# Kernel tuning notes

Measured on AMD Instinct MI355X. Metric: run time of the kernel, lower is better.

## Reference

```python
import jax, jax.numpy as jnp
import numpy as np
import math

L, B, T, C, H, DH, V, MEM = 6, 2, 1024, 1024, 16, 64, 32000, 128

def _ln(x, g, b):
    m = jnp.mean(x, -1, keepdims=True)
    v = jnp.mean((x - m) ** 2, -1, keepdims=True)
    return (x - m) * jax.lax.rsqrt(v + 1e-5) * g + b

def _rel_shift(x):
    # x: [B,H,Q,K]; TransformerXL shift trick: pad zero col, reshape, drop first row
    b, h, q, k = x.shape
    xp = jnp.pad(x, ((0, 0), (0, 0), (0, 0), (1, 0)))
    xp = xp.reshape(b, h, k + 1, q)
    return xp[:, :, 1:, :].reshape(b, h, q, k)

def setup_inputs():
    key = jax.random.key(0)
    ks = jax.random.split(key, 12)
    d = {}
    d['idx'] = jax.random.randint(ks[0], (B, T), 0, V)
    d['mems'] = jax.random.normal(ks[1], (L, B, MEM, C), dtype=jnp.float32) * 0.02
    d['wte'] = jax.random.normal(ks[2], (V, C), dtype=jnp.float32) * 0.02
    d['ln1_g'] = jnp.ones((L, C), jnp.float32); d['ln1_b'] = jnp.zeros((L, C), jnp.float32)
    d['attn_w'] = jax.random.normal(ks[3], (L, C, 3 * C), dtype=jnp.float32) * 0.02
    d['attn_b'] = jnp.zeros((L, 3 * C), jnp.float32)
    d['proj_w'] = jax.random.normal(ks[4], (L, C, C), dtype=jnp.float32) * 0.02
    d['proj_b'] = jnp.zeros((L, C), jnp.float32)
    d['r_emb'] = jax.random.normal(ks[5], (L, H, DH), dtype=jnp.float32) * 0.02
    d['r_bias'] = jax.random.normal(ks[6], (L, H, DH), dtype=jnp.float32) * 0.02
    d['ln2_g'] = jnp.ones((L, C), jnp.float32); d['ln2_b'] = jnp.zeros((L, C), jnp.float32)
    d['fc_w'] = jax.random.normal(ks[7], (L, C, 4 * C), dtype=jnp.float32) * 0.02
    d['fc_b'] = jnp.zeros((L, 4 * C), jnp.float32)
    d['fc2_w'] = jax.random.normal(ks[8], (L, 4 * C, C), dtype=jnp.float32) * 0.02
    d['fc2_b'] = jnp.zeros((L, C), jnp.float32)
    d['lnf_g'] = jnp.ones((C,), jnp.float32); d['lnf_b'] = jnp.zeros((C,), jnp.float32)
    d['lm_w'] = jax.random.normal(ks[9], (C, V), dtype=jnp.float32) * 0.02
    return d

def _attn(x, mem, w, b, pw, pb, remb, rbias):
    Bx, Tx, Cx = x.shape
    cat = jnp.concatenate([mem, x], axis=1)          # [B,K,C], K = mem_len + Tx
    K = cat.shape[1]
    qkv = cat @ w + b
    q, k, v = jnp.split(qkv, 3, axis=-1)
    q = q.reshape(Bx, K, H, DH).transpose(0, 2, 1, 3)
    k = k.reshape(Bx, K, H, DH).transpose(0, 2, 1, 3)
    v = v.reshape(Bx, K, H, DH).transpose(0, 2, 1, 3)
    q = q + rbias[None, :, None, :]
    AC = jnp.einsum('bhid,bhjd->bhij', q, k)
    # BD: r is r_emb broadcast over positions, so q@r^T is constant over j
    s = jnp.einsum('bhid,hd->bhi', q, remb)
    BD = _rel_shift(jnp.broadcast_to(s[..., None], (Bx, H, K, K)))
    p = jax.nn.softmax((AC + BD) / math.sqrt(DH), axis=-1)
    y = jnp.einsum('bhij,bhjd->bhid', p, v).transpose(0, 2, 1, 3).reshape(Bx, K, Cx)
    y = y @ pw + pb
    new_mem = cat[:, -MEM:]
    return y, new_mem

def reference(idx, mems, wte, ln1_g, ln1_b, attn_w, attn_b, proj_w, proj_b, r_emb, r_bias, ln2_g, ln2_b, fc_w, fc_b, fc2_w, fc2_b, lnf_g, lnf_b, lm_w):
    x = wte[idx]                                      # [B,T,C]
    new_mems = []
    for l in range(L):
        h = _ln(x, ln1_g[l], ln1_b[l])
        y, nm = _attn(h, mems[l], attn_w[l], attn_b[l], proj_w[l], proj_b[l], r_emb[l], r_bias[l])
        h2 = _ln(y, ln2_g[l], ln2_b[l])
        m = jax.nn.gelu(h2 @ fc_w[l] + fc_b[l], approximate=False) @ fc2_w[l] + fc2_b[l]
        x = y + m                                     # note: residual onto attn output (length grows by MEM per layer)
        new_mems.append(nm)
    x = _ln(x, lnf_g, lnf_b)
    logits = x @ lm_w                                 # [B, L*MEM+T, V]
    return logits, jnp.stack(new_mems)
```

## Files before the change

### kernel.cpp

```cpp
#include <hip/hip_runtime.h>
#include <hip/hip_bf16.h>
#include <hip/hip_fp16.h>

#define LNUM 6
#define BB 2
#define TT 1024
#define CC 1024
#define HH 16
#define DHH 64
#define VV 32000
#define MM 128

typedef _Float16 f16;
typedef _Float16 f16x8 __attribute__((ext_vector_type(8)));
typedef float f32x4 __attribute__((ext_vector_type(4)));

__device__ __forceinline__ void g2lds16(const void* g, void* l) {
    __builtin_amdgcn_global_load_lds((const __attribute__((address_space(1))) void*)g,
                                     (__attribute__((address_space(3))) void*)l,
                                     16, 0, 0);
}

__device__ __forceinline__ float wred(float v) {
#pragma unroll
    for (int o = 32; o > 0; o >>= 1) v += __shfl_xor(v, o);
    return v;
}

__global__ __launch_bounds__(256)
void transpose_k(const float* __restrict__ W, f16* __restrict__ WT, int R, int Cc)
{
    __shared__ float tile[64][65];
    const size_t base = (size_t)blockIdx.z * R * Cc;
    const int c0 = blockIdx.x * 64, r0 = blockIdx.y * 64;
    const int tx = threadIdx.x & 15, ty = threadIdx.x >> 4;
#pragma unroll
    for (int i = 0; i < 4; ++i) {
        const int row = ty + i * 16;
        float4 v = *(const float4*)&W[base + (size_t)(r0 + row) * Cc + c0 + tx * 4];
        tile[row][tx * 4 + 0] = v.x;
        tile[row][tx * 4 + 1] = v.y;
        tile[row][tx * 4 + 2] = v.z;
        tile[row][tx * 4 + 3] = v.w;
    }
    __syncthreads();
#pragma unroll
    for (int i = 0; i < 4; ++i) {
        const int c = ty + i * 16;
        union { f16 h4[4]; uint2 u; } pk;
        pk.h4[0] = (f16)tile[tx * 4 + 0][c];
        pk.h4[1] = (f16)tile[tx * 4 + 1][c];
        pk.h4[2] = (f16)tile[tx * 4 + 2][c];
        pk.h4[3] = (f16)tile[tx * 4 + 3][c];
        *(uint2*)&WT[base + (size_t)(c0 + c) * R + r0 + tx * 4] = pk.u;
    }
}

__global__ __launch_bounds__(256)
void embed_k(const int* __restrict__ idx, const float* __restrict__ wte, float* __restrict__ X)
{
    const int row = blockIdx.x;
    const int id = idx[row];
    const float4* src = (const float4*)(wte + (size_t)id * CC);
    float4* dst = (float4*)(X + (size_t)row * CC);
    dst[threadIdx.x] = src[threadIdx.x];
}

__global__ __launch_bounds__(256)
void ln_k(const float* __restrict__ X, const float* __restrict__ g,
          const float* __restrict__ bta, f16* __restrict__ outH)
{
    const int row = blockIdx.x * 4 + (threadIdx.x >> 6);
    const int lane = threadIdx.x & 63;
    const float4* xr = (const float4*)(X + (size_t)row * CC);
    float4 v[4];
    float s = 0.f;
#pragma unroll
    for (int i = 0; i < 4; ++i) { v[i] = xr[i * 64 + lane]; s += v[i].x + v[i].y + v[i].z + v[i].w; }
    s = wred(s);
    const float mean = s * (1.f / CC);
    float q = 0.f;
#pragma unroll
    for (int i = 0; i < 4; ++i) {
        float a = v[i].x - mean, b = v[i].y - mean, c = v[i].z - mean, d = v[i].w - mean;
        q += a * a + b * b + c * c + d * d;
    }
    q = wred(q);
    const float rs = rsqrtf(q * (1.f / CC) + 1e-5f);
    const float4* g4 = (const float4*)g;
    const float4* b4 = (const float4*)bta;
    uint2* orow = (uint2*)(outH + (size_t)row * CC);
#pragma unroll
    for (int i = 0; i < 4; ++i) {
        float4 gg = g4[i * 64 + lane], bb = b4[i * 64 + lane];
        union { f16 h4[4]; uint2 u; } pk;
        pk.h4[0] = (f16)((v[i].x - mean) * rs * gg.x + bb.x);
        pk.h4[1] = (f16)((v[i].y - mean) * rs * gg.y + bb.y);
        pk.h4[2] = (f16)((v[i].z - mean) * rs * gg.z + bb.z);
        pk.h4[3] = (f16)((v[i].w - mean) * rs * gg.w + bb.w);
        orow[i * 64 + lane] = pk.u;
    }
}

__global__ __launch_bounds__(256)
void ln1cat_k(const float* __restrict__ X, const float* __restrict__ memsL,
              const float* __restrict__ g, const float* __restrict__ bta,
              f16* __restrict__ catH, float* __restrict__ nmOut,
              int K, int Kin)
{
    const int row = blockIdx.x * 4 + (threadIdx.x >> 6);
    const int lane = threadIdx.x & 63;
    const int b = row / K, rr = row % K;
    uint2* crow = (uint2*)(catH + (size_t)row * CC);
    if (rr < MM) {
        const float4* src = (const float4*)(memsL + ((size_t)b * MM + rr) * CC);
#pragma unroll
        for (int i = 0; i < 4; ++i) {
            float4 vv = src[i * 64 + lane];
            union { f16 h4[4]; uint2 u; } pk;
            pk.h4[0] = (f16)vv.x; pk.h4[1] = (f16)vv.y; pk.h4[2] = (f16)vv.z; pk.h4[3] = (f16)vv.w;
            crow[i * 64 + lane] = pk.u;
        }
        return;
    }
    const float4* xr = (const float4*)(X + ((size_t)b * Kin + (rr - MM)) * CC);
    float4 v[4];
    float s = 0.f;
#pragma unroll
    for (int i = 0; i < 4; ++i) { v[i] = xr[i * 64 + lane]; s += v[i].x + v[i].y + v[i].z + v[i].w; }
    s = wred(s);
    const float mean = s * (1.f / CC);
    float q = 0.f;
#pragma unroll
    for (int i = 0; i < 4; ++i) {
        float a = v[i].x - mean, b2 = v[i].y - mean, c = v[i].z - mean, d = v[i].w - mean;
        q += a * a + b2 * b2 + c * c + d * d;
    }
    q = wred(q);
    const float rs = rsqrtf(q * (1.f / CC) + 1e-5f);
    const float4* g4 = (const float4*)g;
    const float4* b4 = (const float4*)bta;
    float4* nm = nullptr;
    if (rr >= K - MM) nm = (float4*)(nmOut + ((size_t)b * MM + (rr - (K - MM))) * CC);
#pragma unroll
    for (int i = 0; i < 4; ++i) {
        float4 gg = g4[i * 64 + lane], bb = b4[i * 64 + lane];
        float4 o;
        o.x = (v[i].x - mean) * rs * gg.x + bb.x;
        o.y = (v[i].y - mean) * rs * gg.y + bb.y;
        o.z = (v[i].z - mean) * rs * gg.z + bb.z;
        o.w = (v[i].w - mean) * rs * gg.w + bb.w;
        union { f16 h4[4]; uint2 u; } pk;
        pk.h4[0] = (f16)o.x; pk.h4[1] = (f16)o.y; pk.h4[2] = (f16)o.z; pk.h4[3] = (f16)o.w;
        crow[i * 64 + lane] = pk.u;
        if (nm) nm[i * 64 + lane] = o;
    }
}

template <int EPI>
__global__ __launch_bounds__(256, 3)
void gemm_k(const f16* __restrict__ A, const f16* __restrict__ BT,
            const float* __restrict__ bias, const float* __restrict__ res,
            float* __restrict__ outF, f16* __restrict__ outH,
            int M, int N, int Kc)
{
    __shared__ f16 sA[2][128 * 32];
    __shared__ f16 sB[2][128 * 32];

    const int nbn = N >> 7;
    const int nwg = gridDim.x;
    const int id = blockIdx.x;
    const int qq = nwg >> 3, r8 = nwg & 7;
    const int xcd = id & 7, pos = id >> 3;
    const int wgid = (xcd < r8 ? xcd * (qq + 1) : r8 * (qq + 1) + (xcd - r8) * qq) + pos;
    const int bm = wgid / nbn, bn = wgid % nbn;

    const int tid = threadIdx.x;
    const int w = tid >> 6, l = tid & 63;
    const int wr = w >> 1, wc = w & 1;
    const int lr = l & 15, lk = (l >> 4) * 8;

    f32x4 acc[4][4] = {};

    const int ar = w * 32 + (l >> 2);
    const int ak = (l & 3) * 8;
    const f16* gA = A + (size_t)(bm * 128 + ar) * Kc + ak;
    const f16* gB = BT + (size_t)(bn * 128 + ar) * Kc + ak;

    auto stage = [&](int slot, int kt) {
        g2lds16(gA + kt, &sA[slot][w * 1024]);
        g2lds16(gA + kt + (size_t)16 * Kc, &sA[slot][w * 1024 + 512]);
        g2lds16(gB + kt, &sB[slot][w * 1024]);
        g2lds16(gB + kt + (size_t)16 * Kc, &sB[slot][w * 1024 + 512]);
    };

    stage(0, 0);
    asm volatile("s_waitcnt vmcnt(0)" ::: "memory");
    __builtin_amdgcn_s_barrier();

    int cur = 0;
    for (int kt = 0; kt < Kc; kt += 32) {
        if (kt + 32 < Kc) stage(cur ^ 1, kt + 32);
        f16x8 af[4], bf[4];
#pragma unroll
        for (int mi = 0; mi < 4; ++mi) af[mi] = *(const f16x8*)&sA[cur][(wr * 64 + mi * 16 + lr) * 32 + lk];
#pragma unroll
        for (int ni = 0; ni < 4; ++ni) bf[ni] = *(const f16x8*)&sB[cur][(wc * 64 + ni * 16 + lr) * 32 + lk];
        asm volatile("s_waitcnt lgkmcnt(0)" ::: "memory");
        __builtin_amdgcn_sched_barrier(0);
#pragma unroll
        for (int mi = 0; mi < 4; ++mi)
#pragma unroll
            for (int ni = 0; ni < 4; ++ni)
                acc[mi][ni] = __builtin_amdgcn_mfma_f32_16x16x32_f16(af[mi], bf[ni], acc[mi][ni], 0, 0, 0);
        asm volatile("s_waitcnt vmcnt(0)" ::: "memory");
        __builtin_amdgcn_s_barrier();
        cur ^= 1;
    }

    const int orow0 = bm * 128 + wr * 64 + (l >> 4) * 4;
    const int ocol0 = bn * 128 + wc * 64 + lr;
#pragma unroll
    for (int mi = 0; mi < 4; ++mi)
#pragma unroll
        for (int ni = 0; ni < 4; ++ni) {
            const int col = ocol0 + ni * 16;
            const float bv = (EPI >= 1) ? bias[col] : 0.f;
#pragma unroll
            for (int r = 0; r < 4; ++r) {
                const int row = orow0 + mi * 16 + r;
                float v = acc[mi][ni][r] + bv;
                if (EPI == 2) {
                    const float u = 1.5957691216057308f * (v + 0.044715f * v * v * v);
                    const float e = __expf(u);
                    v = v * e / (e + 1.f);
                    outH[(size_t)row * N + col] = (f16)v;
                } else if (EPI == 4) {
                    outH[(size_t)row * N + col] = (f16)v;
                } else if (EPI == 3) {
                    v += res[(size_t)row * N + col];
                    outF[(size_t)row * N + col] = v;
                } else {
                    outF[(size_t)row * N + col] = v;
                }
            }
        }
}

template <int EPI>
__global__ __launch_bounds__(256, 3)
void gemm64_k(const f16* __restrict__ A, const f16* __restrict__ BT,
              const float* __restrict__ bias, const float* __restrict__ res,
              float* __restrict__ outF, f16* __restrict__ outH,
              int M, int N, int Kc)
{
    __shared__ f16 sA[2][128 * 32];
    __shared__ f16 sB[2][64 * 32];

    const int nbn = N >> 6;
    const int nwg = gridDim.x;
    const int id = blockIdx.x;
    const int qq = nwg >> 3, r8 = nwg & 7;
    const int xcd = id & 7, pos = id >> 3;
    const int wgid = (xcd < r8 ? xcd * (qq + 1) : r8 * (qq + 1) + (xcd - r8) * qq) + pos;
    const int bm = wgid / nbn, bn = wgid % nbn;

    const int tid = threadIdx.x;
    const int w = tid >> 6, l = tid & 63;
    const int wr = w >> 1, wc = w & 1;
    const int lr = l & 15, lk = (l >> 4) * 8;

    f32x4 acc[4][2] = {};

    const int ar = w * 32 + (l >> 2);
    const int br = w * 16 + (l >> 2);
    const int ak = (l & 3) * 8;
    const f16* gA = A + (size_t)(bm * 128 + ar) * Kc + ak;
    const f16* gB = BT + (size_t)(bn * 64 + br) * Kc + ak;

    auto stage = [&](int slot, int kt) {
        g2lds16(gA + kt, &sA[slot][w * 1024]);
        g2lds16(gA + kt + (size_t)16 * Kc, &sA[slot][w * 1024 + 512]);
        g2lds16(gB + kt, &sB[slot][w * 512]);
    };

    stage(0, 0);
    asm volatile("s_waitcnt vmcnt(0)" ::: "memory");
    __builtin_amdgcn_s_barrier();

    int cur = 0;
    for (int kt = 0; kt < Kc; kt += 32) {
        if (kt + 32 < Kc) stage(cur ^ 1, kt + 32);
        f16x8 af[4], bf[2];
#pragma unroll
        for (int mi = 0; mi < 4; ++mi) af[mi] = *(const f16x8*)&sA[cur][(wr * 64 + mi * 16 + lr) * 32 + lk];
#pragma unroll
        for (int ni = 0; ni < 2; ++ni) bf[ni] = *(const f16x8*)&sB[cur][(wc * 32 + ni * 16 + lr) * 32 + lk];
        asm volatile("s_waitcnt lgkmcnt(0)" ::: "memory");
        __builtin_amdgcn_sched_barrier(0);
#pragma unroll
        for (int mi = 0; mi < 4; ++mi)
#pragma unroll
            for (int ni = 0; ni < 2; ++ni)
                acc[mi][ni] = __builtin_amdgcn_mfma_f32_16x16x32_f16(af[mi], bf[ni], acc[mi][ni], 0, 0, 0);
        asm volatile("s_waitcnt vmcnt(0)" ::: "memory");
        __builtin_amdgcn_s_barrier();
        cur ^= 1;
    }

    const int orow0 = bm * 128 + wr * 64 + (l >> 4) * 4;
    const int ocol0 = bn * 64 + wc * 32 + lr;
#pragma unroll
    for (int mi = 0; mi < 4; ++mi)
#pragma unroll
        for (int ni = 0; ni < 2; ++ni) {
            const int col = ocol0 + ni * 16;
            const float bv = (EPI >= 1) ? bias[col] : 0.f;
#pragma unroll
            for (int r = 0; r < 4; ++r) {
                const int row = orow0 + mi * 16 + r;
                float v = acc[mi][ni][r] + bv;
                if (EPI == 3) {
                    v += res[(size_t)row * N + col];
                    outF[(size_t)row * N + col] = v;
                } else if (EPI == 4) {
                    outH[(size_t)row * N + col] = (f16)v;
                } else {
                    outF[(size_t)row * N + col] = v;
                }
            }
        }
}

template <int EPI>
__global__ __launch_bounds__(512, 2)
void gemm256_k(const f16* __restrict__ A, const f16* __restrict__ BT,
               const float* __restrict__ bias,
               float* __restrict__ outF, f16* __restrict__ outH,
               int M, int N, int Kc)
{
    __shared__ char ldsbuf[131072];
    char* ldsA = ldsbuf;
    char* ldsB = ldsbuf + 65536;

    const int nbm = M >> 8;
    const int nwg = gridDim.x;
    int id = blockIdx.x;
    const int qq = nwg >> 3, rr8 = nwg & 7;
    const int xcd = id & 7, pos = id >> 3;
    const int wgid = (xcd < rr8 ? xcd * (qq + 1) : rr8 * (qq + 1) + (xcd - rr8) * qq) + pos;
    const int bm = wgid % nbm, bn = wgid / nbm;

    const int t_ = threadIdx.x;
    const int w = t_ >> 6, l = t_ & 63;
    const int wm = w >> 2, wn = w & 3;
    const int lr = l & 15, lhi = l >> 4;

    const f16* gA = A + (size_t)bm * 256 * Kc;
    const f16* gB = BT + (size_t)bn * 256 * Kc;

    auto stage = [&](const f16* Gbase, char* ldsHalf, int kt) {
#pragma unroll
        for (int ii = 0; ii < 2; ++ii) {
            const int gb = (w << 1) + ii;
            const int s = (gb << 6) + l;
            const int row = s >> 3, grp = s & 7;
            g2lds16(Gbase + (size_t)row * Kc + kt + ((grp ^ (row & 7)) << 3),
                    ldsHalf + gb * 1024);
        }
    };
    auto rdfrag = [&](const char* halfBase, int rowInHalf, int ks) -> f16x8 {
        return *(const f16x8*)(halfBase + rowInHalf * 128 +
                               ((((ks << 2) + lhi) ^ (rowInHalf & 7)) << 4));
    };

    f32x4 acc[8][4] = {};
    f16x8 aA[4][2], blo[2][2], bhi[2][2];

    const int NT = Kc >> 6;
    const char* aHalf0 = ldsA + wm * 16384;
    const char* aHalf1 = ldsA + 32768 + wm * 16384;
    const char* bHalf0 = ldsB + (wn >> 1) * 16384;
    const char* bHalf1 = ldsB + 32768 + (wn >> 1) * 16384;
    const int brow = (wn & 1) * 64;

    stage(gA, ldsA + 0, 0);
    stage(gA + (size_t)128 * Kc, ldsA + 16384, 0);
    stage(gB, ldsB + 0, 0);
    stage(gB + (size_t)128 * Kc, ldsB + 16384, 0);
    stage(gB, ldsB + 32768, 64);
    stage(gB + (size_t)128 * Kc, ldsB + 49152, 64);
    asm volatile("s_waitcnt vmcnt(0)" ::: "memory");
    __builtin_amdgcn_s_barrier();

#define MFMA_QUAD(MQ, NQ, BR)                                                            \
    __builtin_amdgcn_s_setprio(1);                                                       \
    _Pragma("unroll") for (int mf = 0; mf < 4; ++mf)                                     \
    _Pragma("unroll") for (int nf = 0; nf < 2; ++nf)                                     \
    _Pragma("unroll") for (int ks = 0; ks < 2; ++ks)                                     \
        acc[(MQ)*4 + mf][(NQ)*2 + nf] =                                                  \
            __builtin_amdgcn_mfma_f32_16x16x32_f16(aA[mf][ks], BR[nf][ks],               \
                                                   acc[(MQ)*4 + mf][(NQ)*2 + nf], 0, 0, 0); \
    __builtin_amdgcn_s_setprio(0);

#define PHASE_SYNC()                                          \
    __builtin_amdgcn_s_barrier();                             \
    asm volatile("s_waitcnt lgkmcnt(0)" ::: "memory");        \
    __builtin_amdgcn_sched_barrier(0);

    for (int t = 0; t < NT; t += 2) {
        const bool pf0 = (t + 2) < NT;
        const int kb = (t + 1) << 6, kc2 = (t + 2) << 6, kd = (t + 3) << 6;

#pragma unroll
        for (int mf = 0; mf < 4; ++mf)
#pragma unroll
            for (int ks = 0; ks < 2; ++ks) aA[mf][ks] = rdfrag(aHalf0, mf * 16 + lr, ks);
#pragma unroll
        for (int nf = 0; nf < 2; ++nf)
#pragma unroll
            for (int ks = 0; ks < 2; ++ks) blo[nf][ks] = rdfrag(bHalf0, brow + nf * 16 + lr, ks);
        stage(gA, ldsA + 32768, kb);
        PHASE_SYNC();
        MFMA_QUAD(0, 0, blo);
        __builtin_amdgcn_s_barrier();

#pragma unroll
        for (int nf = 0; nf < 2; ++nf)
#pragma unroll
            for (int ks = 0; ks < 2; ++ks) bhi[nf][ks] = rdfrag(bHalf0, brow + 32 + nf * 16 + lr, ks);
        stage(gA + (size_t)128 * Kc, ldsA + 49152, kb);
        PHASE_SYNC();
        MFMA_QUAD(0, 1, bhi);
        __builtin_amdgcn_s_barrier();

#pragma unroll
        for (int mf = 0; mf < 4; ++mf)
#pragma unroll
            for (int ks = 0; ks < 2; ++ks) aA[mf][ks] = rdfrag(aHalf0, 64 + mf * 16 + lr, ks);
        if (pf0) stage(gB, ldsB + 0, kc2);
        PHASE_SYNC();
        MFMA_QUAD(1, 0, blo);
        __builtin_amdgcn_s_barrier();

        if (pf0) {
            stage(gB + (size_t)128 * Kc, ldsB + 16384, kc2);
            asm volatile("s_waitcnt vmcnt(4)" ::: "memory");
        } else {
            asm volatile("s_waitcnt vmcnt(0)" ::: "memory");
        }
        PHASE_SYNC();
        MFMA_QUAD(1, 1, bhi);
        __builtin_amdgcn_s_barrier();

#pragma unroll
        for (int mf = 0; mf < 4; ++mf)
#pragma unroll
            for (int ks = 0; ks < 2; ++ks) aA[mf][ks] = rdfrag(aHalf1, mf * 16 + lr, ks);
#pragma unroll
        for (int nf = 0; nf < 2; ++nf)
#pragma unroll
            for (int ks = 0; ks < 2; ++ks) blo[nf][ks] = rdfrag(bHalf1, brow + nf * 16 + lr, ks);
        if (pf0) stage(gA, ldsA + 0, kc2);
        PHASE_SYNC();
        MFMA_QUAD(0, 0, blo);
        __builtin_amdgcn_s_barrier();

#pragma unroll
        for (int nf = 0; nf < 2; ++nf)
#pragma unroll
            for (int ks = 0; ks < 2; ++ks) bhi[nf][ks] = rdfrag(bHalf1, brow + 32 + nf * 16 + lr, ks);
        if (pf0) stage(gA + (size_t)128 * Kc, ldsA + 16384, kc2);
        PHASE_SYNC();
        MFMA_QUAD(0, 1, bhi);
        __builtin_amdgcn_s_barrier();

#pragma unroll
        for (int mf = 0; mf < 4; ++mf)
#pragma unroll
            for (int ks = 0; ks < 2; ++ks) aA[mf][ks] = rdfrag(aHalf1, 64 + mf * 16 + lr, ks);
        if (pf0) stage(gB, ldsB + 32768, kd);
        PHASE_SYNC();
        MFMA_QUAD(1, 0, blo);
        __builtin_amdgcn_s_barrier();

        if (pf0) {
            stage(gB + (size_t)128 * Kc, ldsB + 49152, kd);
            asm volatile("s_waitcnt vmcnt(4)" ::: "memory");
        } else {
            asm volatile("s_waitcnt vmcnt(0)" ::: "memory");
        }
        PHASE_SYNC();
        MFMA_QUAD(1, 1, bhi);
        __builtin_amdgcn_s_barrier();
    }
#undef MFMA_QUAD
#undef PHASE_SYNC

    const int rb0 = bm * 256 + wm * 128 + lhi * 4;
    const int cb0 = bn * 256 + wn * 64 + lr;
#pragma unroll
    for (int mf = 0; mf < 8; ++mf)
#pragma unroll
        for (int nf = 0; nf < 4; ++nf) {
            const int col = cb0 + nf * 16;
            const float bv = (EPI >= 1) ? bias[col] : 0.f;
#pragma unroll
            for (int r = 0; r < 4; ++r) {
                const int row = rb0 + mf * 16 + r;
                float v = acc[mf][nf][r] + bv;
                if (EPI == 2) {
                    const float u = 1.5957691216057308f * (v + 0.044715f * v * v * v);
                    const float e = __expf(u);
                    v = v * e / (e + 1.f);
                    outH[(size_t)row * N + col] = (f16)v;
                } else if (EPI == 4) {
                    outH[(size_t)row * N + col] = (f16)v;
                } else {
                    outF[(size_t)row * N + col] = v;
                }
            }
        }
}

__global__ __launch_bounds__(256)
void attn_k(const f16* __restrict__ qkv, const float* __restrict__ remb,
            const float* __restrict__ rbias, f16* __restrict__ yH, int K)
{
    __shared__ f16 K_lds[2][64 * 64];
    __shared__ f16 Vt_lds[2][64 * 64];
    __shared__ f16 P_lds[64 * 64];
    __shared__ float s_s[66];

    const int b = blockIdx.x >> 4, h = blockIdx.x & 15;
    const int i0 = blockIdx.y * 64;
    const int t = threadIdx.x;
    const int w = t >> 6, l = t & 63;
    const int c = l & 15, g = l >> 4;

    const f16* qg = qkv + (size_t)b * K * 3072 + h * 64;
    const f16* kg = qg + 1024;
    const f16* vg = qg + 2048;
    const float* rb = rbias + h * 64;
    const float* re = remb + h * 64;

    const int kb = t >> 4, db = t & 15;

    auto stageK = [&](int j0, int slot) {
#pragma unroll
        for (int i = 0; i < 2; ++i) {
            const int s = w * 128 + i * 64 + l;
            const int row = s >> 3, grp = s & 7;
            g2lds16(kg + (size_t)(j0 + row) * 3072 + ((grp ^ (row & 7)) * 8),
                    (char*)K_lds[slot] + (size_t)(w * 128 + i * 64) * 16);
        }
    };
    auto loadV = [&](int j0, uint2* rowv) {
#pragma unroll
        for (int i = 0; i < 4; ++i)
            rowv[i] = *(const uint2*)(vg + (size_t)(j0 + kb * 4 + i) * 3072 + db * 4);
    };
    auto writeVt = [&](const uint2* rowvu, int slot) {
#pragma unroll
        for (int j = 0; j < 4; ++j) {
            union { uint2 u; f16 hh[4]; } colv;
#pragma unroll
            for (int i = 0; i < 4; ++i) {
                union { uint2 u; f16 hh[4]; } rv; rv.u = rowvu[i];
                colv.hh[i] = rv.hh[j];
            }
            const int d = db * 4 + j;
            *(uint2*)((char*)Vt_lds[slot] + d * 128 + ((kb * 8) ^ ((d & 7) << 4))) = colv.u;
        }
    };

    f16x8 qf[2];
    {
        const int qrow = i0 + w * 16 + c;
#pragma unroll
        for (int ks = 0; ks < 2; ++ks) {
            f16x8 raw = *(const f16x8*)(qg + (size_t)qrow * 3072 + ks * 32 + g * 8);
            f16x8 o;
#pragma unroll
            for (int j = 0; j < 8; ++j) o[j] = (f16)((float)raw[j] + rb[ks * 32 + g * 8 + j]);
            qf[ks] = o;
        }
    }
    if (t < 65) {
        float sv = 0.f;
        const int i = i0 + t;
        if (i < K) {
            const f16* qr = qg + (size_t)i * 3072;
#pragma unroll
            for (int d8 = 0; d8 < 8; ++d8) {
                f16x8 v8 = *(const f16x8*)(qr + d8 * 8);
#pragma unroll
                for (int j = 0; j < 8; ++j) sv += ((float)v8[j] + rb[d8 * 8 + j]) * re[d8 * 8 + j];
            }
        }
        s_s[t] = sv;
    }

    {
        uint2 rowv[4];
        stageK(0, 0);
        loadV(0, rowv);
        writeVt(rowv, 0);
    }
    __syncthreads();

    float sA[4], sB[4];
#pragma unroll
    for (int r = 0; r < 4; ++r) {
        sA[r] = s_s[w * 16 + g * 4 + r];
        sB[r] = s_s[w * 16 + g * 4 + r + 1];
    }

    float m_run[4] = {0.f, 0.f, 0.f, 0.f};
    float psum[4] = {0.f, 0.f, 0.f, 0.f};
    f32x4 yacc[4] = {};

    int cur = 0;
    for (int j0 = 0; j0 < K; j0 += 64, cur ^= 1) {
        const bool more = (j0 + 64) < K;
        uint2 rowv[4];
        if (more) { stageK(j0 + 64, cur ^ 1); loadV(j0 + 64, rowv); }

        f32x4 sc[4] = {};
#pragma unroll
        for (int tt = 0; tt < 4; ++tt) {
            const int row = tt * 16 + c;
#pragma unroll
            for (int ks = 0; ks < 2; ++ks) {
                f16x8 kf = *(const f16x8*)((char*)K_lds[cur] + row * 128 + ((ks * 64 + g * 16) ^ ((row & 7) << 4)));
                sc[tt] = __builtin_amdgcn_mfma_f32_16x16x32_f16(qf[ks], kf, sc[tt], 0, 0, 0);
            }
        }

        float p[4][4];
#pragma unroll
        for (int tt = 0; tt < 4; ++tt)
#pragma unroll
            for (int r = 0; r < 4; ++r) {
                const int gi = i0 + w * 16 + g * 4 + r;
                const int gj = j0 + tt * 16 + c;
                const float bd = (gj <= gi) ? sA[r] : ((gj == gi + 1) ? 0.f : sB[r]);
                p[tt][r] = (sc[tt][r] + bd) * 0.125f;
            }

        float lmax[4];
        bool need = false;
#pragma unroll
        for (int r = 0; r < 4; ++r) {
            lmax[r] = fmaxf(fmaxf(p[0][r], p[1][r]), fmaxf(p[2][r], p[3][r]));
            need |= (lmax[r] > m_run[r] + 8.f);
        }
        if (__any(need)) {
#pragma unroll
            for (int r = 0; r < 4; ++r) {
                float mx = lmax[r];
                mx = fmaxf(mx, __shfl_xor(mx, 1));
                mx = fmaxf(mx, __shfl_xor(mx, 2));
                mx = fmaxf(mx, __shfl_xor(mx, 4));
                mx = fmaxf(mx, __shfl_xor(mx, 8));
                if (mx > m_run[r]) {
                    const float f = __expf(m_run[r] - mx);
                    m_run[r] = mx;
                    psum[r] *= f;
#pragma unroll
                    for (int tt = 0; tt < 4; ++tt) yacc[tt][r] *= f;
                }
            }
        }
#pragma unroll
        for (int r = 0; r < 4; ++r) {
            float ss = 0.f;
#pragma unroll
            for (int tt = 0; tt < 4; ++tt) {
                const float e = __expf(p[tt][r] - m_run[r]);
                p[tt][r] = e;
                ss += e;
            }
            psum[r] += ss;
        }

        if (more) writeVt(rowv, cur ^ 1);
#pragma unroll
        for (int tt = 0; tt < 4; ++tt)
#pragma unroll
            for (int r = 0; r < 4; ++r) {
                const int q = w * 16 + g * 4 + r;
                *(f16*)((char*)P_lds + q * 128 + (((tt * 16 + c) * 2) ^ ((q & 7) << 4))) = (f16)p[tt][r];
            }
        asm volatile("s_waitcnt lgkmcnt(0)" ::: "memory");
        __builtin_amdgcn_sched_barrier(0);

        {
            const int qrow = w * 16 + c;
            f16x8 pa[2];
#pragma unroll
            for (int ks = 0; ks < 2; ++ks)
                pa[ks] = *(const f16x8*)((char*)P_lds + qrow * 128 + ((ks * 64 + g * 16) ^ ((qrow & 7) << 4)));
#pragma unroll
            for (int tt = 0; tt < 4; ++tt) {
                const int drow = tt * 16 + c;
#pragma unroll
                for (int ks = 0; ks < 2; ++ks) {
                    f16x8 vb = *(const f16x8*)((char*)Vt_lds[cur] + drow * 128 + ((ks * 64 + g * 16) ^ ((drow & 7) << 4)));
                    yacc[tt] = __builtin_amdgcn_mfma_f32_16x16x32_f16(pa[ks], vb, yacc[tt], 0, 0, 0);
                }
            }
        }
        __syncthreads();
    }

#pragma unroll
    for (int r = 0; r < 4; ++r) {
        float ps = psum[r];
        ps += __shfl_xor(ps, 1);
        ps += __shfl_xor(ps, 2);
        ps += __shfl_xor(ps, 4);
        ps += __shfl_xor(ps, 8);
        const float inv = 1.f / ps;
        const int row = i0 + w * 16 + g * 4 + r;
        f16* dst = yH + (size_t)(b * K + row) * CC + h * 64;
#pragma unroll
        for (int tt = 0; tt < 4; ++tt)
            dst[tt * 16 + c] = (f16)(yacc[tt][r] * inv);
    }
}

extern "C" void kernel_launch(void* const* d_in, const int* in_sizes, int n_in,
                              void* d_out, int out_size, void* d_ws, size_t ws_size,
                              hipStream_t stream)
{
    (void)in_sizes; (void)n_in; (void)out_size; (void)ws_size;
    const int*   idx    = (const int*)  d_in[0];
    const float* mems   = (const float*)d_in[1];
    const float* wte    = (const float*)d_in[2];
    const float* ln1_g  = (const float*)d_in[3];
    const float* ln1_b  = (const float*)d_in[4];
    const float* attn_w = (const float*)d_in[5];
    const float* attn_b = (const float*)d_in[6];
    const float* proj_w = (const float*)d_in[7];
    const float* proj_b = (const float*)d_in[8];
    const float* r_emb  = (const float*)d_in[9];
    const float* r_bias = (const float*)d_in[10];
    const float* ln2_g  = (const float*)d_in[11];
    const float* ln2_b  = (const float*)d_in[12];
    const float* fc_w   = (const float*)d_in[13];
    const float* fc_b   = (const float*)d_in[14];
    const float* fc2_w  = (const float*)d_in[15];
    const float* fc2_b  = (const float*)d_in[16];
    const float* lnf_g  = (const float*)d_in[17];
    const float* lnf_b  = (const float*)d_in[18];
    const float* lm_w   = (const float*)d_in[19];
    float* out = (float*)d_out;

    char* wp = (char*)d_ws; size_t off = 0;
    auto carve = [&](size_t bytes) -> void* {
        void* p = wp + off; off += (bytes + 255) & ~(size_t)255; return p;
    };
    const int KMAX = TT + LNUM * MM;
    f16*  attn_wT = (f16*) carve((size_t)LNUM * 3 * CC * CC * 2);
    f16*  proj_wT = (f16*) carve((size_t)LNUM * CC * CC * 2);
    f16*  fc_wT   = (f16*) carve((size_t)LNUM * 4 * CC * CC * 2);
    f16*  fc2_wT  = (f16*) carve((size_t)LNUM * 4 * CC * CC * 2);
    f16*  lm_wT   = (f16*) carve((size_t)VV * CC * 2);
    float* x0     = (float*)carve((size_t)BB * KMAX * CC * 4);
    float* x1     = (float*)carve((size_t)BB * KMAX * CC * 4);
    f16*  catH    = (f16*) carve((size_t)BB * KMAX * CC * 2);
    f16*  qkv16   = (f16*) carve((size_t)BB * KMAX * 3 * CC * 2);
    f16*  yH      = (f16*) carve((size_t)BB * KMAX * CC * 2);
    float* yp     = (float*)carve((size_t)BB * KMAX * CC * 4);
    f16*  h2H     = (f16*) carve((size_t)BB * KMAX * CC * 2);
    f16*  a1H     = (f16*) carve((size_t)BB * KMAX * 4 * CC * 2);
    f16*  xfH     = (f16*) carve((size_t)BB * KMAX * CC * 2);

    transpose_k<<<dim3(3 * CC / 64, CC / 64, LNUM), 256, 0, stream>>>(attn_w, attn_wT, CC, 3 * CC);
    transpose_k<<<dim3(CC / 64, CC / 64, LNUM),     256, 0, stream>>>(proj_w, proj_wT, CC, CC);
    transpose_k<<<dim3(4 * CC / 64, CC / 64, LNUM), 256, 0, stream>>>(fc_w, fc_wT, CC, 4 * CC);
    transpose_k<<<dim3(CC / 64, 4 * CC / 64, LNUM), 256, 0, stream>>>(fc2_w, fc2_wT, 4 * CC, CC);
    transpose_k<<<dim3(VV / 64, CC / 64, 1),        256, 0, stream>>>(lm_w, lm_wT, CC, VV);

    embed_k<<<BB * TT, 256, 0, stream>>>(idx, wte, x0);

    const size_t LOGITS = (size_t)BB * KMAX * VV;
    float* xcur = x0; float* xnxt = x1;
    for (int l = 0; l < LNUM; ++l) {
        const int Kin = TT + MM * l;
        const int K = Kin + MM;
        const int Mrows = BB * K;
        const int nbm128 = Mrows / 128;
        ln1cat_k<<<Mrows / 4, 256, 0, stream>>>(xcur, mems + (size_t)l * BB * MM * CC,
                                                ln1_g + l * CC, ln1_b + l * CC,
                                                catH, out + LOGITS + (size_t)l * BB * MM * CC, K, Kin);
        gemm_k<4><<<(3 * CC / 128) * nbm128, 256, 0, stream>>>(
            catH, attn_wT + (size_t)l * 3 * CC * CC, attn_b + (size_t)l * 3 * CC, nullptr,
            nullptr, qkv16, Mrows, 3 * CC, CC);
        attn_k<<<dim3(BB * HH, K / 64), 256, 0, stream>>>(
            qkv16, r_emb + (size_t)l * HH * DHH, r_bias + (size_t)l * HH * DHH, yH, K);
        gemm64_k<1><<<(CC / 64) * nbm128, 256, 0, stream>>>(
            yH, proj_wT + (size_t)l * CC * CC, proj_b + (size_t)l * CC, nullptr,
            yp, nullptr, Mrows, CC, CC);
        ln_k<<<Mrows / 4, 256, 0, stream>>>(yp, ln2_g + l * CC, ln2_b + l * CC, h2H);
        gemm_k<2><<<(4 * CC / 128) * nbm128, 256, 0, stream>>>(
            h2H, fc_wT + (size_t)l * 4 * CC * CC, fc_b + (size_t)l * 4 * CC, nullptr,
            nullptr, a1H, Mrows, 4 * CC, CC);
        gemm64_k<3><<<(CC / 64) * nbm128, 256, 0, stream>>>(
            a1H, fc2_wT + (size_t)l * 4 * CC * CC, fc2_b + (size_t)l * CC, yp,
            xnxt, nullptr, Mrows, CC, 4 * CC);
        float* tmp = xcur; xcur = xnxt; xnxt = tmp;
    }
    ln_k<<<(BB * KMAX) / 4, 256, 0, stream>>>(xcur, lnf_g, lnf_b, xfH);
    gemm256_k<0><<<(BB * KMAX / 256) * (VV / 256), 512, 0, stream>>>(
        xfH, lm_wT, nullptr, out, nullptr, BB * KMAX, VV, CC);
}
```

Measured before the change: 1.890 ms.

## Process 128 query rows per attention block and use exp2 softmax

After: 2.090 ms. 1.11x slower.

```diff
diff --git a/kernel.cpp b/kernel.cpp
--- a/kernel.cpp
+++ b/kernel.cpp
@@ -509,12 +509,7 @@
             for (int r = 0; r < 4; ++r) {
                 const int row = rb0 + mf * 16 + r;
                 float v = acc[mf][nf][r] + bv;
-                if (EPI == 2) {
-                    const float u = 1.5957691216057308f * (v + 0.044715f * v * v * v);
-                    const float e = __expf(u);
-                    v = v * e / (e + 1.f);
-                    outH[(size_t)row * N + col] = (f16)v;
-                } else if (EPI == 4) {
+                if (EPI == 4) {
                     outH[(size_t)row * N + col] = (f16)v;
                 } else {
                     outF[(size_t)row * N + col] = v;
@@ -529,11 +524,11 @@
 {
     __shared__ f16 K_lds[2][64 * 64];
     __shared__ f16 Vt_lds[2][64 * 64];
-    __shared__ f16 P_lds[64 * 64];
-    __shared__ float s_s[66];
+    __shared__ f16 P_lds[128 * 64];
+    __shared__ float s_s[132];
 
     const int b = blockIdx.x >> 4, h = blockIdx.x & 15;
-    const int i0 = blockIdx.y * 64;
+    const int i0 = blockIdx.y * 128;
     const int t = threadIdx.x;
     const int w = t >> 6, l = t & 63;
     const int c = l & 15, g = l >> 4;
@@ -546,6 +541,8 @@
 
     const int kb = t >> 4, db = t & 15;
 
+    const float SCL = 0.125f * 1.44269504088896f;
+
     auto stageK = [&](int j0, int slot) {
 #pragma unroll
         for (int i = 0; i < 2; ++i) {
@@ -574,19 +571,20 @@
         }
     };
 
-    f16x8 qf[2];
-    {
-        const int qrow = i0 + w * 16 + c;
+    f16x8 qf[2][2];
+#pragma unroll
+    for (int rg = 0; rg < 2; ++rg) {
+        const int qrow = i0 + w * 32 + rg * 16 + c;
 #pragma unroll
         for (int ks = 0; ks < 2; ++ks) {
             f16x8 raw = *(const f16x8*)(qg + (size_t)qrow * 3072 + ks * 32 + g * 8);
             f16x8 o;
 #pragma unroll
             for (int j = 0; j < 8; ++j) o[j] = (f16)((float)raw[j] + rb[ks * 32 + g * 8 + j]);
-            qf[ks] = o;
-        }
-    }
-    if (t < 65) {
+            qf[rg][ks] = o;
+        }
+    }
+    if (t < 130) {
         float sv = 0.f;
         const int i = i0 + t;
         if (i < K) {
@@ -609,16 +607,18 @@
     }
     __syncthreads();
 
-    float sA[4], sB[4];
-#pragma unroll
-    for (int r = 0; r < 4; ++r) {
-        sA[r] = s_s[w * 16 + g * 4 + r];
-        sB[r] = s_s[w * 16 + g * 4 + r + 1];
-    }
-
-    float m_run[4] = {0.f, 0.f, 0.f, 0.f};
-    float psum[4] = {0.f, 0.f, 0.f, 0.f};
-    f32x4 yacc[4] = {};
+    float sA[2][4], sB[2][4];
+#pragma unroll
+    for (int rg = 0; rg < 2; ++rg)
+#pragma unroll
+        for (int r = 0; r < 4; ++r) {
+            sA[rg][r] = s_s[w * 32 + rg * 16 + g * 4 + r];
+            sB[rg][r] = s_s[w * 32 + rg * 16 + g * 4 + r + 1];
+        }
+
+    float m_run[2][4] = {};
+    float psum[2][4] = {};
+    f32x4 yacc[2][4] = {};
 
     int cur = 0;
     for (int j0 = 0; j0 < K; j0 += 64, cur ^= 1) {
@@ -626,88 +626,105 @@
         uint2 rowv[4];
         if (more) { stageK(j0 + 64, cur ^ 1); loadV(j0 + 64, rowv); }
 
-        f32x4 sc[4] = {};
+        f32x4 sc[2][4] = {};
 #pragma unroll
         for (int tt = 0; tt < 4; ++tt) {
             const int row = tt * 16 + c;
 #pragma unroll
             for (int ks = 0; ks < 2; ++ks) {
                 f16x8 kf = *(const f16x8*)((char*)K_lds[cur] + row * 128 + ((ks * 64 + g * 16) ^ ((row & 7) << 4)));
-                sc[tt] = __builtin_amdgcn_mfma_f32_16x16x32_f16(qf[ks], kf, sc[tt], 0, 0, 0);
-            }
-        }
-
-        float p[4][4];
-#pragma unroll
-        for (int tt = 0; tt < 4; ++tt)
+#pragma unroll
+                for (int rg = 0; rg < 2; ++rg)
+                    sc[rg][tt] = __builtin_amdgcn_mfma_f32_16x16x32_f16(qf[rg][ks], kf, sc[rg][tt], 0, 0, 0);
+            }
+        }
+
+        float p[2][4][4];
+#pragma unroll
+        for (int rg = 0; rg < 2; ++rg)
+#pragma unroll
+            for (int tt = 0; tt < 4; ++tt)
+#pragma unroll
+                for (int r = 0; r < 4; ++r) {
+                    const int gi = i0 + w * 32 + rg * 16 + g * 4 + r;
+                    const int gj = j0 + tt * 16 + c;
+                    const float bd = (gj <= gi) ? sA[rg][r] : ((gj == gi + 1) ? 0.f : sB[rg][r]);
+                    p[rg][tt][r] = (sc[rg][tt][r] + bd) * SCL;
+                }
+
+        float lmax[2][4];
+        bool need = false;
+#pragma unroll
+        for (int rg = 0; rg < 2; ++rg)
 #pragma unroll
             for (int r = 0; r < 4; ++r) {
-                const int gi = i0 + w * 16 + g * 4 + r;
-                const int gj = j0 + tt * 16 + c;
-                const float bd = (gj <= gi) ? sA[r] : ((gj == gi + 1) ? 0.f : sB[r]);
-                p[tt][r] = (sc[tt][r] + bd) * 0.125f;
-            }
-
-        float lmax[4];
-        bool need = false;
-#pragma unroll
-        for (int r = 0; r < 4; ++r) {
-            lmax[r] = fmaxf(fmaxf(p[0][r], p[1][r]), fmaxf(p[2][r], p[3][r]));
-            need |= (lmax[r] > m_run[r] + 8.f);
-        }
+                lmax[rg][r] = fmaxf(fmaxf(p[rg][0][r], p[rg][1][r]), fmaxf(p[rg][2][r], p[rg][3][r]));
+                need |= (lmax[rg][r] > m_run[rg][r] + 8.f);
+            }
         if (__any(need)) {
 #pragma unroll
+            for (int rg = 0; rg < 2; ++rg)
+#pragma unroll
+                for (int r = 0; r < 4; ++r) {
+                    float mx = lmax[rg][r];
+                    mx = fmaxf(mx, __shfl_xor(mx, 1));
+                    mx = fmaxf(mx, __shfl_xor(mx, 2));
+                    mx = fmaxf(mx, __shfl_xor(mx, 4));
+                    mx = fmaxf(mx, __shfl_xor(mx, 8));
+                    if (mx > m_run[rg][r]) {
+                        const float f = exp2f(m_run[rg][r] - mx);
+                        m_run[rg][r] = mx;
+                        psum[rg][r] *= f;
+#pragma unroll
+                        for (int tt = 0; tt < 4; ++tt) yacc[rg][tt][r] *= f;
+                    }
+                }
+        }
+#pragma unroll
+        for (int rg = 0; rg < 2; ++rg)
+#pragma unroll
             for (int r = 0; r < 4; ++r) {
-                float mx = lmax[r];
-                mx = fmaxf(mx, __shfl_xor(mx, 1));
-                mx = fmaxf(mx, __shfl_xor(mx, 2));
-                mx = fmaxf(mx, __shfl_xor(mx, 4));
-                mx = fmaxf(mx, __shfl_xor(mx, 8));
-                if (mx > m_run[r]) {
-                    const float f = __expf(m_run[r] - mx);
-                    m_run[r] = mx;
-                    psum[r] *= f;
-#pragma unroll
-                    for (int tt = 0; tt < 4; ++tt) yacc[tt][r] *= f;
+                float ss = 0.f;
+#pragma unroll
+                for (int tt = 0; tt < 4; ++tt) {
+                    const float e = exp2f(p[rg][tt][r] - m_run[rg][r]);
+                    p[rg][tt][r] = e;
+                    ss += e;
                 }
-            }
-        }
-#pragma unroll
-        for (int r = 0; r < 4; ++r) {
-            float ss = 0.f;
-#pragma unroll
-            for (int tt = 0; tt < 4; ++tt) {
-                const float e = __expf(p[tt][r] - m_run[r]);
-                p[tt][r] = e;
-                ss += e;
-            }
-            psum[r] += ss;
-        }
+                psum[rg][r] += ss;
+            }
 
         if (more) writeVt(rowv, cur ^ 1);
 #pragma unroll
-        for (int tt = 0; tt < 4; ++tt)
-#pragma unroll
-            for (int r = 0; r < 4; ++r) {
-                const int q = w * 16 + g * 4 + r;
-                *(f16*)((char*)P_lds + q * 128 + (((tt * 16 + c) * 2) ^ ((q & 7) << 4))) = (f16)p[tt][r];
-            }
+        for (int rg = 0; rg < 2; ++rg)
+#pragma unroll
+            for (int tt = 0; tt < 4; ++tt)
+#pragma unroll
+                for (int r = 0; r < 4; ++r) {
+                    const int q = w * 32 + rg * 16 + g * 4 + r;
+                    *(f16*)((char*)P_lds + q * 128 + (((tt * 16 + c) * 2) ^ ((q & 7) << 4))) = (f16)p[rg][tt][r];
+                }
         asm volatile("s_waitcnt lgkmcnt(0)" ::: "memory");
         __builtin_amdgcn_sched_barrier(0);
 
         {
-            const int qrow = w * 16 + c;
-            f16x8 pa[2];
-#pragma unroll
-            for (int ks = 0; ks < 2; ++ks)
-                pa[ks] = *(const f16x8*)((char*)P_lds + qrow * 128 + ((ks * 64 + g * 16) ^ ((qrow & 7) << 4)));
+            f16x8 pa[2][2];
+#pragma unroll
+            for (int rg = 0; rg < 2; ++rg) {
+                const int qrow = w * 32 + rg * 16 + c;
+#pragma unroll
+                for (int ks = 0; ks < 2; ++ks)
+                    pa[rg][ks] = *(const f16x8*)((char*)P_lds + qrow * 128 + ((ks * 64 + g * 16) ^ ((qrow & 7) << 4)));
+            }
 #pragma unroll
             for (int tt = 0; tt < 4; ++tt) {
                 const int drow = tt * 16 + c;
 #pragma unroll
                 for (int ks = 0; ks < 2; ++ks) {
                     f16x8 vb = *(const f16x8*)((char*)Vt_lds[cur] + drow * 128 + ((ks * 64 + g * 16) ^ ((drow & 7) << 4)));
-                    yacc[tt] = __builtin_amdgcn_mfma_f32_16x16x32_f16(pa[ks], vb, yacc[tt], 0, 0, 0);
+#pragma unroll
+                    for (int rg = 0; rg < 2; ++rg)
+                        yacc[rg][tt] = __builtin_amdgcn_mfma_f32_16x16x32_f16(pa[rg][ks], vb, yacc[rg][tt], 0, 0, 0);
                 }
             }
         }
@@ -715,19 +732,21 @@
     }
 
 #pragma unroll
-    for (int r = 0; r < 4; ++r) {
-        float ps = psum[r];
-        ps += __shfl_xor(ps, 1);
-        ps += __shfl_xor(ps, 2);
-        ps += __shfl_xor(ps, 4);
-        ps += __shfl_xor(ps, 8);
-        const float inv = 1.f / ps;
-        const int row = i0 + w * 16 + g * 4 + r;
-        f16* dst = yH + (size_t)(b * K + row) * CC + h * 64;
-#pragma unroll
-        for (int tt = 0; tt < 4; ++tt)
-            dst[tt * 16 + c] = (f16)(yacc[tt][r] * inv);
-    }
+    for (int rg = 0; rg < 2; ++rg)
+#pragma unroll
+        for (int r = 0; r < 4; ++r) {
+            float ps = psum[rg][r];
+            ps += __shfl_xor(ps, 1);
+            ps += __shfl_xor(ps, 2);
+            ps += __shfl_xor(ps, 4);
+            ps += __shfl_xor(ps, 8);
+            const float inv = 1.f / ps;
+            const int row = i0 + w * 32 + rg * 16 + g * 4 + r;
+            f16* dst = yH + (size_t)(b * K + row) * CC + h * 64;
+#pragma unroll
+            for (int tt = 0; tt < 4; ++tt)
+                dst[tt * 16 + c] = (f16)(yacc[rg][tt][r] * inv);
+        }
 }
 
 extern "C" void kernel_launch(void* const* d_in, const int* in_sizes, int n_in,
@@ -798,7 +817,7 @@
         gemm_k<4><<<(3 * CC / 128) * nbm128, 256, 0, stream>>>(
             catH, attn_wT + (size_t)l * 3 * CC * CC, attn_b + (size_t)l * 3 * CC, nullptr,
             nullptr, qkv16, Mrows, 3 * CC, CC);
-        attn_k<<<dim3(BB * HH, K / 64), 256, 0, stream>>>(
+        attn_k<<<dim3(BB * HH, K / 128), 256, 0, stream>>>(
             qkv16, r_emb + (size_t)l * HH * DHH, r_bias + (size_t)l * HH * DHH, yH, K);
         gemm64_k<1><<<(CC / 64) * nbm128, 256, 0, stream>>>(
             yH, proj_wT + (size_t)l * CC * CC, proj_b + (size_t)l * CC, nullptr,
```
